# Optimization experiments

Measured on AMD Instinct MI355X. Metric: run time of the kernel, lower is better.

## Reference

```python
import jax, jax.numpy as jnp
import numpy as np

N_NODES = 100000
N_EDGES = 1600000
IN_DIM, HID_DIM, OUT_DIM = 256, 64, 64


def gcn_conv(x, src, dst, W, b, n_nodes):
    """PyG GCNConv: D^-1/2 (A + I) D^-1/2 X W + b (self-loops added, deg on dst)."""
    h = x @ W  # [N, D_out]
    ones = jnp.ones(src.shape[0], dtype=h.dtype)
    deg = jax.ops.segment_sum(ones, dst, num_segments=n_nodes) + 1.0  # +1 for self-loop
    dinv = jax.lax.rsqrt(deg)  # deg >= 1, always finite
    norm = dinv[src] * dinv[dst]  # [E]
    # neighbor aggregation (scatter-add) + self-loop contribution
    agg = jax.ops.segment_sum(h[src] * norm[:, None], dst, num_segments=n_nodes)
    agg = agg + h * (dinv * dinv)[:, None]
    return agg + b


def gcn_backbone(x, edge_index, W1, b1, W2, b2, n_nodes):
    src, dst = edge_index[0], edge_index[1]
    h = jax.nn.relu(gcn_conv(x, src, dst, W1, b1, n_nodes))
    h = gcn_conv(h, src, dst, W2, b2, n_nodes)
    return h


def zscore(h):
    # torch .std(0) is unbiased (ddof=1)
    return (h - h.mean(axis=0)) / jnp.std(h, axis=0, ddof=1)


def setup_inputs() -> dict:
    key = jax.random.key(0)
    k = jax.random.split(key, 8)
    x1 = jax.random.normal(k[0], (N_NODES, IN_DIM), dtype=jnp.float32)
    x2 = jax.random.normal(k[1], (N_NODES, IN_DIM), dtype=jnp.float32)
    edge_index1 = jax.random.randint(k[2], (2, N_EDGES), 0, N_NODES, dtype=jnp.int64)
    edge_index2 = jax.random.randint(k[3], (2, N_EDGES), 0, N_NODES, dtype=jnp.int64)
    W1 = jax.random.normal(k[4], (IN_DIM, HID_DIM), dtype=jnp.float32) * (1.0 / np.sqrt(IN_DIM))
    b1 = jnp.zeros((HID_DIM,), dtype=jnp.float32)
    W2 = jax.random.normal(k[5], (HID_DIM, OUT_DIM), dtype=jnp.float32) * (1.0 / np.sqrt(HID_DIM))
    b2 = jnp.zeros((OUT_DIM,), dtype=jnp.float32)
    return {"x1": x1, "edge_index1": edge_index1, "x2": x2, "edge_index2": edge_index2,
            "W1": W1, "b1": b1, "W2": W2, "b2": b2}


def reference(x1, edge_index1, x2, edge_index2, W1, b1, W2, b2):
    h1 = gcn_backbone(x1, edge_index1, W1, b1, W2, b2, N_NODES)
    h2 = gcn_backbone(x2, edge_index2, W1, b1, W2, b2, N_NODES)
    return zscore(h1), zscore(h2)
```

## Files before the change

kernel.cpp:

```cpp
#include <hip/hip_runtime.h>
#include <hip/hip_bf16.h>

#define HD 64
#define CH 8192
#define BKT_SHIFT 10
#define SRC_BITS 17
#define MAXBLK 256

typedef __attribute__((ext_vector_type(8))) short bf16x8;
typedef __attribute__((ext_vector_type(4))) float f32x4;

__device__ inline unsigned short f2bf(float x) {
  unsigned u = __float_as_uint(x);
  unsigned r = u + 0x7FFF + ((u >> 16) & 1);
  return (unsigned short)(r >> 16);
}
__device__ inline float bf2f(unsigned short h) {
  return __uint_as_float(((unsigned)h) << 16);
}

__global__ __launch_bounds__(256) void k_wprep(const float* __restrict__ W1,
                                               const float* __restrict__ W2,
                                               unsigned short* __restrict__ Wf1,
                                               unsigned short* __restrict__ Wf2hi,
                                               unsigned short* __restrict__ Wf2lo) {
  int idx = blockIdx.x * blockDim.x + threadIdx.x;
  if (idx < 256 * 64) {
    int k = idx >> 6, c = idx & 63;
    float w = W1[idx];
    int ks = k >> 5, r = k & 31, h2 = r >> 3, j = r & 7;
    int f = c >> 4, r16c = c & 15;
    int pos = (((ks * 4 + f) * 64) + h2 * 16 + r16c) * 8 + j;
    Wf1[pos] = f2bf(w);
  } else if (idx < 256 * 64 + 64 * 64) {
    int i2 = idx - 256 * 64;
    int k = i2 >> 6, c = i2 & 63;
    float w = W2[i2];
    int ks = k >> 5, r = k & 31, h2 = r >> 3, j = r & 7;
    int f = c >> 4, r16c = c & 15;
    int pos = (((ks * 4 + f) * 64) + h2 * 16 + r16c) * 8 + j;
    unsigned short hi = f2bf(w);
    Wf2hi[pos] = hi;
    Wf2lo[pos] = f2bf(w - bf2f(hi));
  }
}

__global__ __launch_bounds__(256) void k_bin1(const int* __restrict__ src0,
                                              const int* __restrict__ dst0,
                                              const int* __restrict__ src1,
                                              const int* __restrict__ dst1,
                                              int* __restrict__ tmp,
                                              int* __restrict__ counts,
                                              int* __restrict__ offsets,
                                              int NB, int NBLK, int E) {
  __shared__ int hist[128];
  __shared__ int pref[128];
  __shared__ int lofs[128];
  __shared__ int stage[CH];
  const int g = blockIdx.x / NBLK;
  const int blk = blockIdx.x % NBLK;
  const int* __restrict__ src = g ? src1 : src0;
  const int* __restrict__ dst = g ? dst1 : dst0;
  int* __restrict__ tmpg = tmp + (size_t)g * NBLK * CH;
  int* __restrict__ cntg = counts + (size_t)g * NB * NBLK;
  int* __restrict__ offg = offsets + (size_t)g * NB * NBLK;
  const int e0 = blk * CH;
  const int len = min(CH, E - e0);
  const int t = threadIdx.x;

  for (int i = t; i < 128; i += 256) hist[i] = 0;
  __syncthreads();
  int dreg[CH / 256];
#pragma unroll
  for (int it = 0; it < CH / 256; ++it) {
    int i = t + it * 256;
    if (i < len) {
      int d = dst[e0 + i];
      dreg[it] = d;
      atomicAdd(&hist[d >> BKT_SHIFT], 1);
    }
  }
  __syncthreads();
  if (t < 128) pref[t] = hist[t];
  __syncthreads();
  for (int off = 1; off < 128; off <<= 1) {
    int v = 0;
    if (t < 128 && t >= off) v = pref[t - off];
    __syncthreads();
    if (t < 128) pref[t] += v;
    __syncthreads();
  }
  if (t < NB) {
    int ex = pref[t] - hist[t];
    lofs[t] = ex;
    cntg[t * NBLK + blk] = hist[t];
    offg[t * NBLK + blk] = ex;
  }
  __syncthreads();
#pragma unroll
  for (int it = 0; it < CH / 256; ++it) {
    int i = t + it * 256;
    if (i < len) {
      int d = dreg[it], s = src[e0 + i];
      int slot = atomicAdd(&lofs[d >> BKT_SHIFT], 1);
      stage[slot] = ((d & ((1 << BKT_SHIFT) - 1)) << SRC_BITS) | s;
    }
  }
  __syncthreads();
  int nv = len >> 2;
  for (int i = t; i < nv; i += 256) ((int4*)(tmpg + e0))[i] = ((const int4*)stage)[i];
  for (int i = (nv << 2) + t; i < len; i += 256) tmpg[e0 + i] = stage[i];
}

__global__ __launch_bounds__(128) void k_bscan(const int* __restrict__ counts,
                                               int* __restrict__ bucket_base,
                                               int* __restrict__ row_start,
                                               int NB, int NBLK, int N, int E) {
  __shared__ int sh[128];
  const int g = blockIdx.x;
  const int* __restrict__ cntg = counts + (size_t)g * NB * NBLK;
  int* __restrict__ bbg = bucket_base + g * (NB + 1);
  int* __restrict__ rsg = row_start + (size_t)g * (N + 1);
  int t = threadIdx.x;
  int v = 0;
  if (t < NB) {
    const int* p = cntg + t * NBLK;
    for (int i = 0; i < NBLK; ++i) v += p[i];
  }
  sh[t] = v;
  __syncthreads();
  for (int off = 1; off < 128; off <<= 1) {
    int x = (t >= off) ? sh[t - off] : 0;
    __syncthreads();
    sh[t] += x;
    __syncthreads();
  }
  if (t < NB) bbg[t] = sh[t] - v;
  if (t == 0) {
    bbg[NB] = E;
    rsg[N] = E;
  }
}

__global__ __launch_bounds__(1024) void k_bin2m(const int* __restrict__ tmp,
                                                const int* __restrict__ counts,
                                                const int* __restrict__ offsets,
                                                const int* __restrict__ bucket_base,
                                                int* __restrict__ row_start,
                                                float* __restrict__ dinv,
                                                int* __restrict__ recs, int N, int NB,
                                                int NBLK, int E) {
  __shared__ int h[1 << BKT_SHIFT];
  __shared__ int lcur[1 << BKT_SHIFT];
  __shared__ int scnt[MAXBLK], soff[MAXBLK];
  const int g = blockIdx.x / NB;
  const int b = blockIdx.x % NB;
  const int* __restrict__ tmpg = tmp + (size_t)g * NBLK * CH;
  const int* __restrict__ cntg = counts + (size_t)g * NB * NBLK;
  const int* __restrict__ offg = offsets + (size_t)g * NB * NBLK;
  const int* __restrict__ bbg = bucket_base + g * (NB + 1);
  int* __restrict__ rsg = row_start + (size_t)g * (N + 1);
  float* __restrict__ dig = dinv + (size_t)g * N;
  int* __restrict__ recg = recs + (size_t)g * E;
  const int t = threadIdx.x;
  const int node0 = b << BKT_SHIFT;
  const int lane = t & 63, w = t >> 6;

  h[t] = 0;
  for (int i = t; i < NBLK; i += 1024) {
    scnt[i] = cntg[b * NBLK + i];
    soff[i] = offg[b * NBLK + i];
  }
  __syncthreads();
  for (int blk = w; blk < NBLK; blk += 16) {
    int cnt = scnt[blk];
    const int* p = tmpg + blk * CH + soff[blk];
    for (int j = lane; j < cnt; j += 64) atomicAdd(&h[p[j] >> SRC_BITS], 1);
  }
  __syncthreads();
  int deg = h[t];
  __syncthreads();
  for (int off = 1; off < 1024; off <<= 1) {
    int x = (t >= off) ? h[t - off] : 0;
    __syncthreads();
    h[t] += x;
    __syncthreads();
  }
  int base = bbg[b] + h[t] - deg;
  lcur[t] = base;
  int n = node0 + t;
  if (n < N) {
    rsg[n] = base;
    dig[n] = rsqrtf((float)deg + 1.0f);
  }
  __syncthreads();
  for (int blk = w; blk < NBLK; blk += 16) {
    int cnt = scnt[blk];
    const int* p = tmpg + blk * CH + soff[blk];
    for (int j = lane; j < cnt; j += 64) {
      int rec = p[j];
      int d = rec >> SRC_BITS;
      int s = rec & ((1 << SRC_BITS) - 1);
      int slot = atomicAdd(&lcur[d], 1);
      recg[slot] = s;
    }
  }
}

template <int K, int A_BF16, int B_LO>
__global__ __launch_bounds__(512) void k_gemm(const void* __restrict__ Xv0,
                                              const void* __restrict__ Xv1,
                                              const unsigned short* __restrict__ Wfh,
                                              const unsigned short* __restrict__ Wfl,
                                              unsigned short* __restrict__ Hb, int N,
                                              int gPer) {
  constexpr int NKS = K / 32;
  const int tid = threadIdx.x;
  const int g = blockIdx.x / gPer;
  const int bblk = blockIdx.x % gPer;
  const void* __restrict__ Xv = g ? Xv1 : Xv0;

  const int lane = tid & 63;
  const int wv = tid >> 6;
  const int r16 = lane & 15;
  const int half = lane >> 4;
  const int row = bblk * 128 + wv * 16 + r16;
  const int rowc = min(row, N - 1);

  f32x4 acc[4];
#pragma unroll
  for (int f = 0; f < 4; ++f) acc[f] = (f32x4){0.f, 0.f, 0.f, 0.f};

#pragma unroll
  for (int ks = 0; ks < NKS; ++ks) {
    bf16x8 ahi;
    if constexpr (A_BF16) {
      union { uint4 u; bf16x8 v; } au;
      au.u = *(const uint4*)((const unsigned short*)Xv + (size_t)rowc * K + ks * 32 + half * 8);
      ahi = au.v;
    } else {
      const float* xp = (const float*)Xv + (size_t)rowc * K + ks * 32 + half * 8;
      float4 a0 = *(const float4*)xp;
      float4 a1 = *(const float4*)(xp + 4);
      union { __hip_bfloat162 h[4]; bf16x8 v; } cu;
      cu.h[0] = __float22bfloat162_rn(make_float2(a0.x, a0.y));
      cu.h[1] = __float22bfloat162_rn(make_float2(a0.z, a0.w));
      cu.h[2] = __float22bfloat162_rn(make_float2(a1.x, a1.y));
      cu.h[3] = __float22bfloat162_rn(make_float2(a1.z, a1.w));
      ahi = cu.v;
    }
#pragma unroll
    for (int f = 0; f < 4; ++f) {
      bf16x8 bh = *(const bf16x8*)&Wfh[(((ks * 4 + f) * 64) + lane) * 8];
      acc[f] = __builtin_amdgcn_mfma_f32_16x16x32_bf16(ahi, bh, acc[f], 0, 0, 0);
      if constexpr (B_LO) {
        bf16x8 bl = *(const bf16x8*)&Wfl[(((ks * 4 + f) * 64) + lane) * 8];
        acc[f] = __builtin_amdgcn_mfma_f32_16x16x32_bf16(ahi, bl, acc[f], 0, 0, 0);
      }
    }
  }

  const int orow0 = bblk * 128 + wv * 16 + half * 4;
#pragma unroll
  for (int f = 0; f < 4; ++f) {
#pragma unroll
    for (int rg = 0; rg < 4; ++rg) {
      int orow = orow0 + rg;
      if (orow < N) Hb[((size_t)g * N + orow) * HD + f * 16 + r16] = f2bf(acc[f][rg]);
    }
  }
}

template <int OUTBF16>
__global__ __launch_bounds__(256) void k_agg(const unsigned short* __restrict__ Hb,
                                             const int* __restrict__ recs,
                                             const int* __restrict__ row_start,
                                             const float* __restrict__ dinv,
                                             const float* __restrict__ bias,
                                             void* __restrict__ outv, int N, int E,
                                             int relu) {
  const int t = threadIdx.x;
  const int nglob = (blockIdx.x * blockDim.x + t) >> 4;
  const int lane16 = t & 15;
  if (nglob >= 2 * N) return;
  const int g = nglob >= N;
  const int node = nglob - g * N;
  const int* __restrict__ rsg = row_start + (size_t)g * (N + 1);
  const int* __restrict__ R = recs + (size_t)g * E;
  const float* __restrict__ dig = dinv + (size_t)g * N;
  const unsigned short* __restrict__ Hbg = Hb + (size_t)g * N * HD;

  const int c0 = lane16 * 4;
  float di = dig[node];
  float a0, a1, a2, a3;
  {
    uint2 h = *(const uint2*)&Hbg[(size_t)node * HD + c0];
    float dd = di * di;
    a0 = bf2f((unsigned short)(h.x & 0xffff)) * dd;
    a1 = bf2f((unsigned short)(h.x >> 16)) * dd;
    a2 = bf2f((unsigned short)(h.y & 0xffff)) * dd;
    a3 = bf2f((unsigned short)(h.y >> 16)) * dd;
  }
  const int beg = rsg[node], end = rsg[node + 1];
  int e = beg;
  for (; e + 8 <= end; e += 8) {
    int s[8];
    uint2 gg[8];
    float n[8];
#pragma unroll
    for (int j = 0; j < 8; ++j) s[j] = R[e + j];
#pragma unroll
    for (int j = 0; j < 8; ++j) {
      gg[j] = *(const uint2*)&Hbg[(size_t)s[j] * HD + c0];
      n[j] = dig[s[j]];
    }
#pragma unroll
    for (int j = 0; j < 8; ++j) {
      float nn = n[j] * di;
      a0 = fmaf(bf2f((unsigned short)(gg[j].x & 0xffff)), nn, a0);
      a1 = fmaf(bf2f((unsigned short)(gg[j].x >> 16)), nn, a1);
      a2 = fmaf(bf2f((unsigned short)(gg[j].y & 0xffff)), nn, a2);
      a3 = fmaf(bf2f((unsigned short)(gg[j].y >> 16)), nn, a3);
    }
  }
  for (; e < end; ++e) {
    int s = R[e];
    uint2 gg = *(const uint2*)&Hbg[(size_t)s * HD + c0];
    float nn = dig[s] * di;
    a0 = fmaf(bf2f((unsigned short)(gg.x & 0xffff)), nn, a0);
    a1 = fmaf(bf2f((unsigned short)(gg.x >> 16)), nn, a1);
    a2 = fmaf(bf2f((unsigned short)(gg.y & 0xffff)), nn, a2);
    a3 = fmaf(bf2f((unsigned short)(gg.y >> 16)), nn, a3);
  }
  float4 bv = *(const float4*)&bias[c0];
  a0 += bv.x; a1 += bv.y; a2 += bv.z; a3 += bv.w;
  if (relu) {
    a0 = fmaxf(a0, 0.f); a1 = fmaxf(a1, 0.f);
    a2 = fmaxf(a2, 0.f); a3 = fmaxf(a3, 0.f);
  }
  if (OUTBF16) {
    uint2 o;
    o.x = ((unsigned)f2bf(a1) << 16) | f2bf(a0);
    o.y = ((unsigned)f2bf(a3) << 16) | f2bf(a2);
    *(uint2*)&((unsigned short*)outv)[(size_t)nglob * HD + c0] = o;
  } else {
    *(float4*)&((float*)outv)[(size_t)nglob * HD + c0] = make_float4(a0, a1, a2, a3);
  }
}


__global__ void k_colstats(const float* __restrict__ H, float* __restrict__ stats, int N,
                           int gridPer) {
  __shared__ float ss[256], sq[256];
  const int g = blockIdx.x / gridPer;
  const int blk = blockIdx.x % gridPer;
  const float* __restrict__ Hg = H + (size_t)g * N * HD;
  float* __restrict__ st = stats + g * 128;
  int t = threadIdx.x;
  int col = t & 63, grp = t >> 6;
  float s = 0.f, q = 0.f;
  for (int row = blk * 4 + grp; row < N; row += gridPer * 4) {
    float v = Hg[(size_t)row * HD + col];
    s += v;
    q += v * v;
  }
  ss[t] = s;
  sq[t] = q;
  __syncthreads();
  if (t < 64) {
    s = ss[t] + ss[t + 64] + ss[t + 128] + ss[t + 192];
    q = sq[t] + sq[t + 64] + sq[t + 128] + sq[t + 192];
    atomicAdd(&st[t], s);
    atomicAdd(&st[64 + t], q);
  }
}

__global__ void k_normalize(float* __restrict__ H, const float* __restrict__ stats, int N) {
  int i = blockIdx.x * blockDim.x + threadIdx.x;
  int total = 2 * N * HD;
  if (i >= total) return;
  int col = i & 63;
  const float* st = stats + (i >= N * HD ? 128 : 0);
  float sum = st[col], sumsq = st[64 + col];
  float mean = sum / (float)N;
  float var = (sumsq - sum * sum / (float)N) / (float)(N - 1);
  float r = rsqrtf(var);
  H[i] = (H[i] - mean) * r;
}


extern "C" void kernel_launch(void* const* d_in, const int* in_sizes, int n_in,
                              void* d_out, int out_size, void* d_ws, size_t ws_size,
                              hipStream_t stream) {
  const int IN_DIM = 256;
  const float* X1 = (const float*)d_in[0];
  const float* X2 = (const float*)d_in[2];
  const int* EI1 = (const int*)d_in[1];
  const int* EI2 = (const int*)d_in[3];
  const float* W1 = (const float*)d_in[4];
  const float* b1 = (const float*)d_in[5];
  const float* W2 = (const float*)d_in[6];
  const float* b2 = (const float*)d_in[7];
  const int N = in_sizes[0] / IN_DIM;
  const int E = in_sizes[1] / 2;
  const int NB = (N + (1 << BKT_SHIFT) - 1) >> BKT_SHIFT;
  const int NBLK = (E + CH - 1) / CH;

  char* ws = (char*)d_ws;
  size_t off = 0;
  auto carve = [&](size_t bytes) -> char* {
    char* p = ws + off;
    off += (bytes + 255) & ~(size_t)255;
    return p;
  };
  unsigned short* Hb = (unsigned short*)carve((size_t)2 * N * HD * 2);
  int* tmp = (int*)carve((size_t)2 * NBLK * CH * 4);
  int* recs = (int*)carve((size_t)2 * E * 4);
  char* zero_base = carve(256 * 4);
  float* stats = (float*)zero_base;
  int* row_start = (int*)carve((size_t)2 * (N + 1) * 4);
  float* dinv = (float*)carve((size_t)2 * N * 4);
  int* bucket_base = (int*)carve((size_t)2 * (NB + 1) * 4);
  int* counts = (int*)carve((size_t)2 * NB * NBLK * 4);
  int* offsets = (int*)carve((size_t)2 * NB * NBLK * 4);
  unsigned short* Wf1 = (unsigned short*)carve(256 * 64 * 2);
  unsigned short* Wf2hi = (unsigned short*)carve(64 * 64 * 2);
  unsigned short* Wf2lo = (unsigned short*)carve(64 * 64 * 2);
  unsigned short* bufAgg = (unsigned short*)d_out;
  (void)ws_size; (void)n_in; (void)out_size;

  const int T = 256;
  const int gPer1 = (N + 127) / 128;
  const int gPer2 = (2 * N + 127) / 128;
  const int gAgg = (2 * N * 16 + T - 1) / T;
  const int gCS = 512;
  const int gElem = (2 * N * HD + T - 1) / T;
  const int gWp = (256 * 64 + 64 * 64 + T - 1) / T;

  (void)hipMemsetAsync(zero_base, 0, 256 * 4, stream);
  k_wprep<<<gWp, T, 0, stream>>>(W1, W2, Wf1, Wf2hi, Wf2lo);
  k_bin1<<<2 * NBLK, T, 0, stream>>>(EI1, EI1 + E, EI2, EI2 + E, tmp, counts, offsets,
                                     NB, NBLK, E);
  k_bscan<<<2, 128, 0, stream>>>(counts, bucket_base, row_start, NB, NBLK, N, E);
  k_bin2m<<<2 * NB, 1024, 0, stream>>>(tmp, counts, offsets, bucket_base, row_start,
                                       dinv, recs, N, NB, NBLK, E);

  k_gemm<256, 0, 0><<<2 * gPer1, 512, 0, stream>>>(X1, X2, Wf1, nullptr, Hb, N, gPer1);
  k_agg<1><<<gAgg, T, 0, stream>>>(Hb, recs, row_start, dinv, b1, bufAgg, N, E, 1);
  k_gemm<64, 1, 1><<<gPer2, 512, 0, stream>>>(bufAgg, bufAgg, Wf2hi, Wf2lo, Hb, 2 * N, gPer2);
  k_agg<0><<<gAgg, T, 0, stream>>>(Hb, recs, row_start, dinv, b2, d_out, N, E, 0);

  k_colstats<<<2 * gCS, T, 0, stream>>>((float*)d_out, stats, N, gCS);
  k_normalize<<<gElem, T, 0, stream>>>((float*)d_out, stats, N);
}
```

Measured before the change: 379.8 us.

## Stage GEMM A-tiles via global_load_lds into swizzled LDS with double buffering

Replaces the templated GEMM with two specialized kernels that load the A operand directly from global memory into XOR-swizzled LDS using global_load_lds. The first-layer GEMM double-buffers 64-column chunks so loads overlap the MFMA work, and both kernels now use 64-row tiles with 256 threads. The aim is more coalesced, better-overlapped loads of the large fp32 X input, replacing per-lane strided vector loads. In exchange it adds LDS traffic and barriers, and the smaller tiles launch more blocks.

```diff
diff --git a/kernel.cpp b/kernel.cpp
--- a/kernel.cpp
+++ b/kernel.cpp
@@ -9,6 +9,13 @@
 
 typedef __attribute__((ext_vector_type(8))) short bf16x8;
 typedef __attribute__((ext_vector_type(4))) float f32x4;
+
+typedef __attribute__((address_space(1))) const unsigned int* gas_ptr;
+typedef __attribute__((address_space(3))) unsigned int* las_ptr;
+
+__device__ inline void gl_lds16(const void* g, void* l) {
+  __builtin_amdgcn_global_load_lds((gas_ptr)g, (las_ptr)l, 16, 0, 0);
+}
 
 __device__ inline unsigned short f2bf(float x) {
   unsigned u = __float_as_uint(x);
@@ -207,66 +214,125 @@
   }
 }
 
-template <int K, int A_BF16, int B_LO>
-__global__ __launch_bounds__(512) void k_gemm(const void* __restrict__ Xv0,
-                                              const void* __restrict__ Xv1,
-                                              const unsigned short* __restrict__ Wfh,
-                                              const unsigned short* __restrict__ Wfl,
-                                              unsigned short* __restrict__ Hb, int N,
-                                              int gPer) {
-  constexpr int NKS = K / 32;
+__global__ __launch_bounds__(256) void k_gemm1(const float* __restrict__ X0,
+                                               const float* __restrict__ X1,
+                                               const unsigned short* __restrict__ Wf1,
+                                               unsigned short* __restrict__ Hb, int N,
+                                               int gPer) {
+  __shared__ float sA[2][64 * 64];
   const int tid = threadIdx.x;
   const int g = blockIdx.x / gPer;
   const int bblk = blockIdx.x % gPer;
-  const void* __restrict__ Xv = g ? Xv1 : Xv0;
-
+  const float* __restrict__ Xv = g ? X1 : X0;
+  const int row0 = bblk * 64;
   const int lane = tid & 63;
   const int wv = tid >> 6;
   const int r16 = lane & 15;
   const int half = lane >> 4;
-  const int row = bblk * 128 + wv * 16 + r16;
-  const int rowc = min(row, N - 1);
+  const int rowL = wv * 16 + r16;
+
+  auto STAGE = [&](int b, int c) {
+#pragma unroll
+    for (int i = 0; i < 4; ++i) {
+      int slot = tid + i * 256;
+      int r = slot >> 4, u = slot & 15;
+      int su = (u & 8) | ((u & 7) ^ (r & 7));
+      int gr = min(row0 + r, N - 1);
+      gl_lds16(Xv + (size_t)gr * 256 + c * 64 + su * 4, (char*)&sA[b][0] + slot * 16);
+    }
+  };
 
   f32x4 acc[4];
 #pragma unroll
   for (int f = 0; f < 4; ++f) acc[f] = (f32x4){0.f, 0.f, 0.f, 0.f};
 
-#pragma unroll
-  for (int ks = 0; ks < NKS; ++ks) {
-    bf16x8 ahi;
-    if constexpr (A_BF16) {
-      union { uint4 u; bf16x8 v; } au;
-      au.u = *(const uint4*)((const unsigned short*)Xv + (size_t)rowc * K + ks * 32 + half * 8);
-      ahi = au.v;
-    } else {
-      const float* xp = (const float*)Xv + (size_t)rowc * K + ks * 32 + half * 8;
-      float4 a0 = *(const float4*)xp;
-      float4 a1 = *(const float4*)(xp + 4);
+  STAGE(0, 0);
+  for (int c = 0; c < 4; ++c) {
+    const int buf = c & 1;
+    if (c < 3) STAGE(buf ^ 1, c + 1);
+    __syncthreads();
+#pragma unroll
+    for (int ks2 = 0; ks2 < 2; ++ks2) {
+      const int ksg = c * 2 + ks2;
+      int v0 = ks2 * 8 + half * 2;
+      int p0 = (v0 & 8) | ((v0 & 7) ^ (rowL & 7));
+      int p1 = ((v0 + 1) & 8) | (((v0 + 1) & 7) ^ (rowL & 7));
+      float4 a0 = *(const float4*)((const char*)&sA[buf][0] + (rowL * 16 + p0) * 16);
+      float4 a1 = *(const float4*)((const char*)&sA[buf][0] + (rowL * 16 + p1) * 16);
       union { __hip_bfloat162 h[4]; bf16x8 v; } cu;
       cu.h[0] = __float22bfloat162_rn(make_float2(a0.x, a0.y));
       cu.h[1] = __float22bfloat162_rn(make_float2(a0.z, a0.w));
       cu.h[2] = __float22bfloat162_rn(make_float2(a1.x, a1.y));
       cu.h[3] = __float22bfloat162_rn(make_float2(a1.z, a1.w));
-      ahi = cu.v;
-    }
-#pragma unroll
-    for (int f = 0; f < 4; ++f) {
-      bf16x8 bh = *(const bf16x8*)&Wfh[(((ks * 4 + f) * 64) + lane) * 8];
-      acc[f] = __builtin_amdgcn_mfma_f32_16x16x32_bf16(ahi, bh, acc[f], 0, 0, 0);
-      if constexpr (B_LO) {
-        bf16x8 bl = *(const bf16x8*)&Wfl[(((ks * 4 + f) * 64) + lane) * 8];
-        acc[f] = __builtin_amdgcn_mfma_f32_16x16x32_bf16(ahi, bl, acc[f], 0, 0, 0);
+      bf16x8 ahi = cu.v;
+#pragma unroll
+      for (int f = 0; f < 4; ++f) {
+        bf16x8 bh = *(const bf16x8*)&Wf1[(((ksg * 4 + f) * 64) + lane) * 8];
+        acc[f] = __builtin_amdgcn_mfma_f32_16x16x32_bf16(ahi, bh, acc[f], 0, 0, 0);
       }
     }
-  }
-
-  const int orow0 = bblk * 128 + wv * 16 + half * 4;
+    __syncthreads();
+  }
+
+  const int orow0 = row0 + wv * 16 + half * 4;
 #pragma unroll
   for (int f = 0; f < 4; ++f) {
 #pragma unroll
     for (int rg = 0; rg < 4; ++rg) {
       int orow = orow0 + rg;
       if (orow < N) Hb[((size_t)g * N + orow) * HD + f * 16 + r16] = f2bf(acc[f][rg]);
+    }
+  }
+}
+
+__global__ __launch_bounds__(256) void k_gemm2(const unsigned short* __restrict__ Xb,
+                                               const unsigned short* __restrict__ Wfh,
+                                               const unsigned short* __restrict__ Wfl,
+                                               unsigned short* __restrict__ Hb, int M) {
+  __shared__ unsigned short sA[64 * 64];
+  const int tid = threadIdx.x;
+  const int row0 = blockIdx.x * 64;
+  const int lane = tid & 63;
+  const int wv = tid >> 6;
+  const int r16 = lane & 15;
+  const int half = lane >> 4;
+  const int rowL = wv * 16 + r16;
+
+#pragma unroll
+  for (int i = 0; i < 2; ++i) {
+    int slot = tid + i * 256;
+    int r = slot >> 3, u = slot & 7;
+    int su = u ^ (r & 7);
+    int gr = min(row0 + r, M - 1);
+    gl_lds16(Xb + (size_t)gr * 64 + su * 8, (char*)sA + slot * 16);
+  }
+  __syncthreads();
+
+  f32x4 acc[4];
+#pragma unroll
+  for (int f = 0; f < 4; ++f) acc[f] = (f32x4){0.f, 0.f, 0.f, 0.f};
+
+#pragma unroll
+  for (int ks = 0; ks < 2; ++ks) {
+    int v = ks * 4 + half;
+    int p = v ^ (rowL & 7);
+    bf16x8 ahi = *(const bf16x8*)((const char*)sA + (rowL * 8 + p) * 16);
+#pragma unroll
+    for (int f = 0; f < 4; ++f) {
+      bf16x8 bh = *(const bf16x8*)&Wfh[(((ks * 4 + f) * 64) + lane) * 8];
+      bf16x8 bl = *(const bf16x8*)&Wfl[(((ks * 4 + f) * 64) + lane) * 8];
+      acc[f] = __builtin_amdgcn_mfma_f32_16x16x32_bf16(ahi, bh, acc[f], 0, 0, 0);
+      acc[f] = __builtin_amdgcn_mfma_f32_16x16x32_bf16(ahi, bl, acc[f], 0, 0, 0);
+    }
+  }
+
+  const int orow0 = row0 + wv * 16 + half * 4;
+#pragma unroll
+  for (int f = 0; f < 4; ++f) {
+#pragma unroll
+    for (int rg = 0; rg < 4; ++rg) {
+      int orow = orow0 + rg;
+      if (orow < M) Hb[(size_t)orow * HD + f * 16 + r16] = f2bf(acc[f][rg]);
     }
   }
 }
@@ -430,8 +496,8 @@
   (void)ws_size; (void)n_in; (void)out_size;
 
   const int T = 256;
-  const int gPer1 = (N + 127) / 128;
-  const int gPer2 = (2 * N + 127) / 128;
+  const int gPer1 = (N + 63) / 64;
+  const int gG2 = (2 * N + 63) / 64;
   const int gAgg = (2 * N * 16 + T - 1) / T;
   const int gCS = 512;
   const int gElem = (2 * N * HD + T - 1) / T;
@@ -445,9 +511,9 @@
   k_bin2m<<<2 * NB, 1024, 0, stream>>>(tmp, counts, offsets, bucket_base, row_start,
                                        dinv, recs, N, NB, NBLK, E);
 
-  k_gemm<256, 0, 0><<<2 * gPer1, 512, 0, stream>>>(X1, X2, Wf1, nullptr, Hb, N, gPer1);
+  k_gemm1<<<2 * gPer1, T, 0, stream>>>(X1, X2, Wf1, Hb, N, gPer1);
   k_agg<1><<<gAgg, T, 0, stream>>>(Hb, recs, row_start, dinv, b1, bufAgg, N, E, 1);
-  k_gemm<64, 1, 1><<<gPer2, 512, 0, stream>>>(bufAgg, bufAgg, Wf2hi, Wf2lo, Hb, 2 * N, gPer2);
+  k_gemm2<<<gG2, T, 0, stream>>>(bufAgg, Wf2hi, Wf2lo, Hb, 2 * N);
   k_agg<0><<<gAgg, T, 0, stream>>>(Hb, recs, row_start, dinv, b2, d_out, N, E, 0);
 
   k_colstats<<<2 * gCS, T, 0, stream>>>((float*)d_out, stats, N, gCS);
```

Result: faster. 363.9 us (-4.2%).
